# Kernel tuning notes

Measured on AMD Instinct MI355X. Metric: run time of the kernel, lower is better.

Reference implementation:

```python
import jax, jax.numpy as jnp
import numpy as np

GROUP_SIZE = 128


def setup_inputs() -> dict:
    key = jax.random.key(0)
    k0, k1, k2, k3 = jax.random.split(key, 4)
    B, S, I, O, G = 4, 2048, 4096, 11008, GROUP_SIZE
    x = jax.random.normal(k0, (B, S, I), dtype=jnp.float32)
    # int4 values in [-8, 7]
    qweight = jax.random.randint(k1, (O, I), -8, 8, dtype=jnp.int32)
    # group-wise positive scales, shape [O, I // G]
    scales = jax.random.uniform(k2, (O, I // G), dtype=jnp.float32,
                                minval=1e-3, maxval=2e-2)
    bias = jax.random.normal(k3, (O,), dtype=jnp.float32) * 0.01
    return {"x": x, "qweight": qweight, "scales": scales, "bias": bias}


def reference(x, qweight, scales, bias):
    # bits == 4, quantized path: group-wise dequant then linear
    O, I = qweight.shape
    G = GROUP_SIZE
    w = qweight.reshape(O, I // G, G).astype(x.dtype) * scales[:, :, None].astype(x.dtype)
    w = w.reshape(O, I)  # dequantized weight [O, I]
    # F.linear: y = x @ w.T + bias
    return jnp.einsum('bsi,oi->bso', x, w) + bias.astype(x.dtype)
```

## Files before the change

### kernel.cpp

```cpp
#include <hip/hip_runtime.h>
#include <hip/hip_bf16.h>


typedef __bf16 bf16_t;
typedef __bf16 bf16x8 __attribute__((ext_vector_type(8)));
typedef float f32x4 __attribute__((ext_vector_type(4)));
typedef int ix4 __attribute__((ext_vector_type(4)));
typedef __attribute__((address_space(3))) unsigned char lds_byte;
typedef __attribute__((address_space(1))) unsigned char gmem_byte;

__global__ void prep_kernel(const float* __restrict__ x, int* __restrict__ xq,
                            float* __restrict__ sx,
                            const int* __restrict__ qw, const float* __restrict__ sc,
                            float* __restrict__ tw, int* __restrict__ wq,
                            int M, int I, int NG) {
  __shared__ float red[256];
  const int b = blockIdx.x;
  const int t = threadIdx.x;
  if (b < M) {
    const float* row = x + (size_t)b * I;
    float mx = 0.f;
    for (int c = t * 4; c < I; c += 1024) {
      const float4 f = *reinterpret_cast<const float4*>(row + c);
      mx = fmaxf(mx, fmaxf(fmaxf(fabsf(f.x), fabsf(f.y)), fmaxf(fabsf(f.z), fabsf(f.w))));
    }
    red[t] = mx;
    __syncthreads();
#pragma unroll
    for (int s = 128; s > 0; s >>= 1) {
      if (t < s) red[t] = fmaxf(red[t], red[t + s]);
      __syncthreads();
    }
    const float rm = fmaxf(red[0], 1e-30f);
    if (t == 0) sx[b] = rm * (1.f / 127.f);
    const float inv = 127.f / rm;
    int* orow = xq + (size_t)b * (I >> 2);
    for (int c = t * 4; c < I; c += 1024) {
      const float4 f = *reinterpret_cast<const float4*>(row + c);
      const int b0 = (int)rintf(f.x * inv), b1 = (int)rintf(f.y * inv);
      const int b2 = (int)rintf(f.z * inv), b3 = (int)rintf(f.w * inv);
      orow[c >> 2] = (b0 & 255) | ((b1 & 255) << 8) | ((b2 & 255) << 16) | (b3 << 24);
    }
  } else {
    const int n = b - M;
    const float* srow = sc + (size_t)n * NG;
    float mx = 0.f;
    for (int g = t; g < NG; g += 256) mx = fmaxf(mx, srow[g]);
    red[t] = mx;
    __syncthreads();
#pragma unroll
    for (int s = 128; s > 0; s >>= 1) {
      if (t < s) red[t] = fmaxf(red[t], red[t + s]);
      __syncthreads();
    }
    const float tn = fmaxf(red[0], 1e-30f) * (8.f / 127.f);
    if (t == 0) tw[n] = tn;
    const float itn = 1.f / tn;
    const int* qrow = qw + (size_t)n * I;
    int* orow = wq + (size_t)n * (I >> 2);
    for (int k0 = t * 16; k0 < I; k0 += 4096) {
      const float f = srow[k0 >> 7] * itn;
      const int4* p = reinterpret_cast<const int4*>(qrow + k0);
      const int4 q0 = p[0], q1 = p[1], q2 = p[2], q3 = p[3];
      int v[16];
      v[0] = (int)rintf((float)q0.x * f); v[1] = (int)rintf((float)q0.y * f);
      v[2] = (int)rintf((float)q0.z * f); v[3] = (int)rintf((float)q0.w * f);
      v[4] = (int)rintf((float)q1.x * f); v[5] = (int)rintf((float)q1.y * f);
      v[6] = (int)rintf((float)q1.z * f); v[7] = (int)rintf((float)q1.w * f);
      v[8] = (int)rintf((float)q2.x * f); v[9] = (int)rintf((float)q2.y * f);
      v[10] = (int)rintf((float)q2.z * f); v[11] = (int)rintf((float)q2.w * f);
      v[12] = (int)rintf((float)q3.x * f); v[13] = (int)rintf((float)q3.y * f);
      v[14] = (int)rintf((float)q3.z * f); v[15] = (int)rintf((float)q3.w * f);
      int4 o;
      o.x = (v[0] & 255) | ((v[1] & 255) << 8) | ((v[2] & 255) << 16) | (v[3] << 24);
      o.y = (v[4] & 255) | ((v[5] & 255) << 8) | ((v[6] & 255) << 16) | (v[7] << 24);
      o.z = (v[8] & 255) | ((v[9] & 255) << 8) | ((v[10] & 255) << 16) | (v[11] << 24);
      o.w = (v[12] & 255) | ((v[13] & 255) << 8) | ((v[14] & 255) << 16) | (v[15] << 24);
      *reinterpret_cast<int4*>(orow + (k0 >> 2)) = o;
    }
  }
}


#define WAITV(n) asm volatile("s_waitcnt vmcnt(" #n ")" ::: "memory")
#define WAITL(n) asm volatile("s_waitcnt lgkmcnt(" #n ")" ::: "memory")
#define BAR() __builtin_amdgcn_s_barrier()
#define SETP(n) __builtin_amdgcn_s_setprio(n)

#define RD_A(DB, q) do { \
  _Pragma("unroll") \
  for (int i_ = 0; i_ < 4; ++i_) { \
    aF[i_][0] = *reinterpret_cast<const ix4*>(&ldsb[(DB) + aRd + (unsigned)((q) * 64 + i_ * 16) * 128u + ks0]); \
    aF[i_][1] = *reinterpret_cast<const ix4*>(&ldsb[(DB) + aRd + (unsigned)((q) * 64 + i_ * 16) * 128u + ks1]); \
  } \
} while (0)

#define RD_B(DB, nh, BF) do { \
  _Pragma("unroll") \
  for (int j_ = 0; j_ < 2; ++j_) { \
    BF[j_][0] = *reinterpret_cast<const ix4*>(&ldsb[(DB) + bRd + (unsigned)((nh) * 32 + j_ * 16) * 128u + ks0]); \
    BF[j_][1] = *reinterpret_cast<const ix4*>(&ldsb[(DB) + bRd + (unsigned)((nh) * 32 + j_ * 16) * 128u + ks1]); \
  } \
} while (0)

#define STG(BASE, P, tau) do { \
  __builtin_amdgcn_global_load_lds((const gmem_byte*)((P) + (size_t)(tau) * 128), \
                                   (lds_byte*)&ldsb[(BASE) + wOff], 16, 0, 0); \
  __builtin_amdgcn_global_load_lds((const gmem_byte*)((P) + (size_t)64 * K + (size_t)(tau) * 128), \
                                   (lds_byte*)&ldsb[(BASE) + 8192u + wOff], 16, 0, 0); \
} while (0)

#define MMQI(q, nh, BF) do { \
  _Pragma("unroll") \
  for (int i_ = 0; i_ < 4; ++i_) \
  _Pragma("unroll") \
  for (int j_ = 0; j_ < 2; ++j_) { \
    acc[(q) * 4 + i_][(nh) * 2 + j_] = __builtin_amdgcn_mfma_i32_16x16x64_i8(aF[i_][0], BF[j_][0], acc[(q) * 4 + i_][(nh) * 2 + j_], 0, 0, 0); \
    acc[(q) * 4 + i_][(nh) * 2 + j_] = __builtin_amdgcn_mfma_i32_16x16x64_i8(aF[i_][1], BF[j_][1], acc[(q) * 4 + i_][(nh) * 2 + j_], 0, 0, 0); \
  } \
} while (0)

__launch_bounds__(512, 2)
__global__ void gemm256_i8_kernel(const char* __restrict__ A, const char* __restrict__ B,
                                  const float* __restrict__ sx, const float* __restrict__ tw,
                                  const float* __restrict__ bias, float* __restrict__ C,
                                  int M, int N, int K) {
  __shared__ __align__(16) unsigned char ldsb[131072];

  const int tid = threadIdx.x;
  const int lane = tid & 63;
  const int w = tid >> 6;
  const int wr = w >> 2;
  const int wc = w & 3;

  const int MT = M >> 8;
  int mt, nt;
  const int bid = blockIdx.x;
  if ((MT & 7) == 0) {
    const int xcd = bid & 7, idx = bid >> 3;
    const int mpx = MT >> 3;
    nt = idx / mpx;
    mt = xcd * mpx + (idx - nt * mpx);
  } else {
    mt = bid % MT;
    nt = bid / MT;
  }
  const int m0 = mt << 8, n0 = nt << 8;

  const int srow8 = lane >> 3;
  const int scol16 = (lane & 7) ^ (srow8 & 7);
  const char* aP0 = A + (size_t)(m0 + w * 8 + srow8) * K + scol16 * 16;
  const char* aP1 = aP0 + (size_t)128 * K;
  const char* bP0 = B + (size_t)(n0 + w * 8 + srow8) * K + scol16 * 16;
  const char* bP1 = bP0 + (size_t)128 * K;
  const unsigned wOff = (unsigned)w * 1024u;

  const unsigned fr = lane & 15;
  const unsigned hi16 = (unsigned)lane >> 4;
  const unsigned sw_ = (fr & 7u) << 4;
  const unsigned ks0 = (hi16 * 16u) ^ sw_;
  const unsigned ks1 = (64u + hi16 * 16u) ^ sw_;
  const unsigned aRd = (unsigned)wr * 16384u + fr * 128u;
  const unsigned bRd = 32768u + (unsigned)(wc >> 1) * 16384u +
                       ((unsigned)(wc & 1) * 64u + fr) * 128u;

  ix4 acc[8][4];
#pragma unroll
  for (int i = 0; i < 8; ++i)
#pragma unroll
    for (int j = 0; j < 4; ++j) acc[i][j] = (ix4){0, 0, 0, 0};

  ix4 aF[4][2], bF0[2][2], bF1[2][2];

  const int NITER = K >> 8;

  STG(0u, aP0, 0); STG(16384u, aP1, 0); STG(32768u, bP0, 0); STG(49152u, bP1, 0);
  STG(98304u, bP0, 1); STG(114688u, bP1, 1);
  WAITV(4);
  BAR();

  for (int it = 0; it < NITER - 1; ++it) {
    const int t = 2 * it;
    RD_A(0u, 0); RD_B(0u, 0, bF0); RD_B(0u, 1, bF1);
    STG(65536u, aP0, t + 1); STG(81920u, aP1, t + 1);
    BAR(); WAITL(4);
    SETP(1); MMQI(0, 0, bF0); SETP(0);
    WAITL(0);
    SETP(1); MMQI(0, 1, bF1); SETP(0); BAR();
    RD_A(0u, 1);
    STG(32768u, bP0, t + 2); STG(49152u, bP1, t + 2);
    WAITV(4);
    BAR(); WAITL(0);
    SETP(1); MMQI(1, 0, bF0); MMQI(1, 1, bF1); SETP(0); BAR();
    RD_A(65536u, 0); RD_B(65536u, 0, bF0); RD_B(65536u, 1, bF1);
    STG(0u, aP0, t + 2); STG(16384u, aP1, t + 2);
    BAR(); WAITL(4);
    SETP(1); MMQI(0, 0, bF0); SETP(0);
    WAITL(0);
    SETP(1); MMQI(0, 1, bF1); SETP(0); BAR();
    RD_A(65536u, 1);
    STG(98304u, bP0, t + 3); STG(114688u, bP1, t + 3);
    WAITV(4);
    BAR(); WAITL(0);
    SETP(1); MMQI(1, 0, bF0); MMQI(1, 1, bF1); SETP(0); BAR();
  }
  {
    RD_A(0u, 0); RD_B(0u, 0, bF0); RD_B(0u, 1, bF1);
    STG(65536u, aP0, 2 * NITER - 1); STG(81920u, aP1, 2 * NITER - 1);
    BAR(); WAITL(4);
    SETP(1); MMQI(0, 0, bF0); SETP(0);
    WAITL(0);
    SETP(1); MMQI(0, 1, bF1); SETP(0); BAR();
    RD_A(0u, 1);
    WAITV(0);
    BAR(); WAITL(0);
    SETP(1); MMQI(1, 0, bF0); MMQI(1, 1, bF1); SETP(0); BAR();
    RD_A(65536u, 0); RD_B(65536u, 0, bF0); RD_B(65536u, 1, bF1);
    WAITL(4);
    SETP(1); MMQI(0, 0, bF0); SETP(0);
    WAITL(0);
    SETP(1); MMQI(0, 1, bF1); SETP(0);
    RD_A(65536u, 1);
    WAITL(0);
    SETP(1); MMQI(1, 0, bF0); MMQI(1, 1, bF1); SETP(0);
  }

  const int row0 = m0 + wr * 128 + ((lane >> 4) << 2);
  const int col0 = n0 + wc * 64 + (lane & 15);
  float sxc[8][4];
#pragma unroll
  for (int hi = 0; hi < 8; ++hi) {
    const int rbase = row0 + (hi >> 2) * 64 + (hi & 3) * 16;
#pragma unroll
    for (int r = 0; r < 4; ++r) sxc[hi][r] = sx[rbase + r];
  }
#pragma unroll
  for (int j = 0; j < 4; ++j) {
    const int n = col0 + j * 16;
    const float tn = tw[n];
    const float bv = bias[n];
#pragma unroll
    for (int hi = 0; hi < 8; ++hi) {
      const int rbase = row0 + (hi >> 2) * 64 + (hi & 3) * 16;
#pragma unroll
      for (int r = 0; r < 4; ++r)
        C[(size_t)(rbase + r) * N + n] = sxc[hi][r] * tn * (float)acc[hi][j][r] + bv;
    }
  }
}

__global__ void cvt_x_kernel(const float* __restrict__ x, bf16_t* __restrict__ xb, long n8) {
  const long stride = (long)gridDim.x * blockDim.x;
  for (long i = (long)blockIdx.x * blockDim.x + threadIdx.x; i < n8; i += stride) {
    const float4* p = reinterpret_cast<const float4*>(x + i * 8);
    const float4 f0 = p[0];
    const float4 f1 = p[1];
    bf16x8 o;
    o[0] = (bf16_t)f0.x; o[1] = (bf16_t)f0.y; o[2] = (bf16_t)f0.z; o[3] = (bf16_t)f0.w;
    o[4] = (bf16_t)f1.x; o[5] = (bf16_t)f1.y; o[6] = (bf16_t)f1.z; o[7] = (bf16_t)f1.w;
    *reinterpret_cast<bf16x8*>(xb + i * 8) = o;
  }
}

__global__ void deq_w_kernel(const int* __restrict__ qw, const float* __restrict__ sc,
                             bf16_t* __restrict__ wb, int I, int G) {
  const int n = blockIdx.y;
  const int kb = blockIdx.x * blockDim.x + threadIdx.x;
  const int k = kb * 8;
  if (k >= I) return;
  const float s = sc[(size_t)n * (I / G) + k / G];
  const int4* qp = reinterpret_cast<const int4*>(qw + (size_t)n * I + k);
  const int4 q0 = qp[0];
  const int4 q1 = qp[1];
  bf16x8 o;
  o[0] = (bf16_t)((float)q0.x * s);
  o[1] = (bf16_t)((float)q0.y * s);
  o[2] = (bf16_t)((float)q0.z * s);
  o[3] = (bf16_t)((float)q0.w * s);
  o[4] = (bf16_t)((float)q1.x * s);
  o[5] = (bf16_t)((float)q1.y * s);
  o[6] = (bf16_t)((float)q1.z * s);
  o[7] = (bf16_t)((float)q1.w * s);
  *reinterpret_cast<bf16x8*>(wb + (size_t)n * I + k) = o;
}

#define BM 128
#define BK 32
__launch_bounds__(256)
__global__ void gemm_bt_kernel(const bf16_t* __restrict__ A, const bf16_t* __restrict__ B,
                               const float* __restrict__ bias, float* __restrict__ C,
                               int M, int N, int K) {
  __shared__ __align__(16) bf16_t As[2][BM * BK];
  __shared__ __align__(16) bf16_t Bs[2][BM * BK];
  const int tid = threadIdx.x;
  const int lane = tid & 63;
  const int w = tid >> 6;
  const int wr = w >> 1;
  const int wc = w & 1;
  const int m0 = blockIdx.y * BM;
  const int n0 = blockIdx.x * BM;
  const int srow = lane >> 2;
  const int schunk = lane & 3;
  f32x4 acc[4][4];
  const f32x4 zero = {0.f, 0.f, 0.f, 0.f};
#pragma unroll
  for (int i = 0; i < 4; ++i)
#pragma unroll
    for (int j = 0; j < 4; ++j) acc[i][j] = zero;
  const int nt = K / BK;
  auto stage = [&](int t, int buf) {
    const int k0 = t * BK;
#pragma unroll
    for (int j = 0; j < 2; ++j) {
      const int row = w * 32 + j * 16;
      const bf16_t* ga = A + (size_t)(m0 + row + srow) * K + k0 + schunk * 8;
      __builtin_amdgcn_global_load_lds((const gmem_byte*)ga, (lds_byte*)&As[buf][row * BK], 16, 0, 0);
      const bf16_t* gb = B + (size_t)(n0 + row + srow) * K + k0 + schunk * 8;
      __builtin_amdgcn_global_load_lds((const gmem_byte*)gb, (lds_byte*)&Bs[buf][row * BK], 16, 0, 0);
    }
  };
  auto compute = [&](int buf) {
    bf16x8 af[4], bfr[4];
    const int fr2 = lane & 15;
    const int kc = (lane >> 4) * 8;
#pragma unroll
    for (int i = 0; i < 4; ++i) {
      af[i] = *reinterpret_cast<const bf16x8*>(&As[buf][(wr * 64 + i * 16 + fr2) * BK + kc]);
      bfr[i] = *reinterpret_cast<const bf16x8*>(&Bs[buf][(wc * 64 + i * 16 + fr2) * BK + kc]);
    }
#pragma unroll
    for (int i = 0; i < 4; ++i)
#pragma unroll
      for (int j = 0; j < 4; ++j)
        acc[i][j] = __builtin_amdgcn_mfma_f32_16x16x32_bf16(af[i], bfr[j], acc[i][j], 0, 0, 0);
  };
  stage(0, 0);
  __syncthreads();
  int cur = 0;
  for (int t = 0; t < nt - 1; ++t) {
    stage(t + 1, cur ^ 1);
    compute(cur);
    __syncthreads();
    cur ^= 1;
  }
  compute(cur);
#pragma unroll
  for (int j = 0; j < 4; ++j) {
    const int n = n0 + wc * 64 + j * 16 + (lane & 15);
    const float bv = bias[n];
#pragma unroll
    for (int i = 0; i < 4; ++i) {
      const int mbase = m0 + wr * 64 + i * 16 + (lane >> 4) * 4;
#pragma unroll
      for (int r = 0; r < 4; ++r)
        C[(size_t)(mbase + r) * N + n] = acc[i][j][r] + bv;
    }
  }
}

extern "C" void kernel_launch(void* const* d_in, const int* in_sizes, int n_in,
                              void* d_out, int out_size, void* d_ws, size_t ws_size,
                              hipStream_t stream) {
  const float* x = (const float*)d_in[0];
  const int* qw = (const int*)d_in[1];
  const float* sc = (const float*)d_in[2];
  const float* bias = (const float*)d_in[3];
  float* out = (float*)d_out;

  const long O = in_sizes[3];
  const long I = in_sizes[1] / O;
  const long M = in_sizes[0] / I;
  const long G = I / (in_sizes[2] / O);
  const long NG = I / G;

  const size_t i8need = (size_t)(M + O) * I + 4 * (size_t)(M + O);
  const bool i8ok = ((M & 255) == 0) && ((O & 255) == 0) && ((I & 255) == 0) &&
                    (G == 128) && ((I >> 8) >= 2) &&
                    (ws_size >= i8need);
  if (i8ok) {
    char* xq = (char*)d_ws;
    char* wq = xq + (size_t)M * I;
    float* sx = (float*)(wq + (size_t)O * I);
    float* tw = sx + M;
    prep_kernel<<<(unsigned)(M + O), 256, 0, stream>>>(x, (int*)xq, sx, qw, sc, tw,
                                                       (int*)wq, (int)M, (int)I, (int)NG);
    const int nwg = (int)((M >> 8) * (O >> 8));
    gemm256_i8_kernel<<<nwg, 512, 0, stream>>>(xq, wq, sx, tw, bias, out, (int)M, (int)O, (int)I);
  } else {
    bf16_t* xb = (bf16_t*)d_ws;
    bf16_t* wb = xb + (size_t)M * I;
    if (ws_size < (size_t)(M + O) * I * sizeof(bf16_t)) return;
    cvt_x_kernel<<<2048, 256, 0, stream>>>(x, xb, M * I / 8);
    dim3 dgrid((unsigned)((I / 8 + 255) / 256), (unsigned)O);
    deq_w_kernel<<<dgrid, 256, 0, stream>>>(qw, sc, wb, (int)I, (int)G);
    dim3 ggrid((unsigned)(O / BM), (unsigned)(M / BM));
    gemm_bt_kernel<<<ggrid, 256, 0, stream>>>(xb, wb, bias, out, (int)M, (int)O, (int)I);
  }
}
```

Before: 487.3 us.

## Shrink int8 GEMM tile to 128x128 with simpler double-buffered pipeline

Replaces the 256x256 output tile int8 MFMA GEMM with a 128x128 tile. Each of 8 waves now computes 32x64, LDS drops to 64KB, and launch bounds allow 4 blocks per CU. The staged split-phase schedule becomes a plain two-buffer ping-pong over 128-wide K chunks. This aims to raise occupancy and simplify synchronisation, but it lowers arithmetic intensity per LDS read and global load.

```diff
diff --git a/kernel.cpp b/kernel.cpp
--- a/kernel.cpp
+++ b/kernel.cpp
@@ -87,19 +87,16 @@
 #define BAR() __builtin_amdgcn_s_barrier()
 #define SETP(n) __builtin_amdgcn_s_setprio(n)
 
-#define RD_A(DB, q) do { \
+#define RD_T(DB) do { \
   _Pragma("unroll") \
-  for (int i_ = 0; i_ < 4; ++i_) { \
-    aF[i_][0] = *reinterpret_cast<const ix4*>(&ldsb[(DB) + aRd + (unsigned)((q) * 64 + i_ * 16) * 128u + ks0]); \
-    aF[i_][1] = *reinterpret_cast<const ix4*>(&ldsb[(DB) + aRd + (unsigned)((q) * 64 + i_ * 16) * 128u + ks1]); \
+  for (int m_ = 0; m_ < 2; ++m_) { \
+    aF[m_][0] = *reinterpret_cast<const ix4*>(&ldsb[(DB) + aRd + (unsigned)(m_ * 16) * 128u + ks0]); \
+    aF[m_][1] = *reinterpret_cast<const ix4*>(&ldsb[(DB) + aRd + (unsigned)(m_ * 16) * 128u + ks1]); \
   } \
-} while (0)
-
-#define RD_B(DB, nh, BF) do { \
   _Pragma("unroll") \
-  for (int j_ = 0; j_ < 2; ++j_) { \
-    BF[j_][0] = *reinterpret_cast<const ix4*>(&ldsb[(DB) + bRd + (unsigned)((nh) * 32 + j_ * 16) * 128u + ks0]); \
-    BF[j_][1] = *reinterpret_cast<const ix4*>(&ldsb[(DB) + bRd + (unsigned)((nh) * 32 + j_ * 16) * 128u + ks1]); \
+  for (int n_ = 0; n_ < 4; ++n_) { \
+    bF[n_][0] = *reinterpret_cast<const ix4*>(&ldsb[(DB) + 16384u + bRd + (unsigned)(n_ * 16) * 128u + ks0]); \
+    bF[n_][1] = *reinterpret_cast<const ix4*>(&ldsb[(DB) + 16384u + bRd + (unsigned)(n_ * 16) * 128u + ks1]); \
   } \
 } while (0)
 
@@ -110,30 +107,30 @@
                                    (lds_byte*)&ldsb[(BASE) + 8192u + wOff], 16, 0, 0); \
 } while (0)
 
-#define MMQI(q, nh, BF) do { \
+#define MM_T() do { \
   _Pragma("unroll") \
-  for (int i_ = 0; i_ < 4; ++i_) \
+  for (int m_ = 0; m_ < 2; ++m_) \
   _Pragma("unroll") \
-  for (int j_ = 0; j_ < 2; ++j_) { \
-    acc[(q) * 4 + i_][(nh) * 2 + j_] = __builtin_amdgcn_mfma_i32_16x16x64_i8(aF[i_][0], BF[j_][0], acc[(q) * 4 + i_][(nh) * 2 + j_], 0, 0, 0); \
-    acc[(q) * 4 + i_][(nh) * 2 + j_] = __builtin_amdgcn_mfma_i32_16x16x64_i8(aF[i_][1], BF[j_][1], acc[(q) * 4 + i_][(nh) * 2 + j_], 0, 0, 0); \
+  for (int n_ = 0; n_ < 4; ++n_) { \
+    acc[m_][n_] = __builtin_amdgcn_mfma_i32_16x16x64_i8(aF[m_][0], bF[n_][0], acc[m_][n_], 0, 0, 0); \
+    acc[m_][n_] = __builtin_amdgcn_mfma_i32_16x16x64_i8(aF[m_][1], bF[n_][1], acc[m_][n_], 0, 0, 0); \
   } \
 } while (0)
 
-__launch_bounds__(512, 2)
-__global__ void gemm256_i8_kernel(const char* __restrict__ A, const char* __restrict__ B,
+__launch_bounds__(512, 4)
+__global__ void gemm128_i8_kernel(const char* __restrict__ A, const char* __restrict__ B,
                                   const float* __restrict__ sx, const float* __restrict__ tw,
                                   const float* __restrict__ bias, float* __restrict__ C,
                                   int M, int N, int K) {
-  __shared__ __align__(16) unsigned char ldsb[131072];
+  __shared__ __align__(16) unsigned char ldsb[65536];
 
   const int tid = threadIdx.x;
   const int lane = tid & 63;
   const int w = tid >> 6;
-  const int wr = w >> 2;
-  const int wc = w & 3;
-
-  const int MT = M >> 8;
+  const int wr = w >> 1;
+  const int wc = w & 1;
+
+  const int MT = M >> 7;
   int mt, nt;
   const int bid = blockIdx.x;
   if ((MT & 7) == 0) {
@@ -145,14 +142,12 @@
     mt = bid % MT;
     nt = bid / MT;
   }
-  const int m0 = mt << 8, n0 = nt << 8;
+  const int m0 = mt << 7, n0 = nt << 7;
 
   const int srow8 = lane >> 3;
   const int scol16 = (lane & 7) ^ (srow8 & 7);
-  const char* aP0 = A + (size_t)(m0 + w * 8 + srow8) * K + scol16 * 16;
-  const char* aP1 = aP0 + (size_t)128 * K;
-  const char* bP0 = B + (size_t)(n0 + w * 8 + srow8) * K + scol16 * 16;
-  const char* bP1 = bP0 + (size_t)128 * K;
+  const char* aP = A + (size_t)(m0 + w * 8 + srow8) * K + scol16 * 16;
+  const char* bP = B + (size_t)(n0 + w * 8 + srow8) * K + scol16 * 16;
   const unsigned wOff = (unsigned)w * 1024u;
 
   const unsigned fr = lane & 15;
@@ -160,91 +155,72 @@
   const unsigned sw_ = (fr & 7u) << 4;
   const unsigned ks0 = (hi16 * 16u) ^ sw_;
   const unsigned ks1 = (64u + hi16 * 16u) ^ sw_;
-  const unsigned aRd = (unsigned)wr * 16384u + fr * 128u;
-  const unsigned bRd = 32768u + (unsigned)(wc >> 1) * 16384u +
-                       ((unsigned)(wc & 1) * 64u + fr) * 128u;
-
-  ix4 acc[8][4];
-#pragma unroll
-  for (int i = 0; i < 8; ++i)
+  const unsigned aRd = ((unsigned)(wr * 32) + fr) * 128u;
+  const unsigned bRd = ((unsigned)(wc * 64) + fr) * 128u;
+
+  ix4 acc[2][4];
+#pragma unroll
+  for (int i = 0; i < 2; ++i)
 #pragma unroll
     for (int j = 0; j < 4; ++j) acc[i][j] = (ix4){0, 0, 0, 0};
 
-  ix4 aF[4][2], bF0[2][2], bF1[2][2];
-
-  const int NITER = K >> 8;
-
-  STG(0u, aP0, 0); STG(16384u, aP1, 0); STG(32768u, bP0, 0); STG(49152u, bP1, 0);
-  STG(98304u, bP0, 1); STG(114688u, bP1, 1);
+  ix4 aF[2][2], bF[4][2];
+
+  const int NITER = K >> 7;
+
+  STG(0u, aP, 0); STG(16384u, bP, 0);
+  STG(32768u, aP, 1); STG(49152u, bP, 1);
   WAITV(4);
   BAR();
 
-  for (int it = 0; it < NITER - 1; ++it) {
+  for (int it = 0; it < (NITER >> 1) - 1; ++it) {
     const int t = 2 * it;
-    RD_A(0u, 0); RD_B(0u, 0, bF0); RD_B(0u, 1, bF1);
-    STG(65536u, aP0, t + 1); STG(81920u, aP1, t + 1);
-    BAR(); WAITL(4);
-    SETP(1); MMQI(0, 0, bF0); SETP(0);
+    RD_T(0u);
     WAITL(0);
-    SETP(1); MMQI(0, 1, bF1); SETP(0); BAR();
-    RD_A(0u, 1);
-    STG(32768u, bP0, t + 2); STG(49152u, bP1, t + 2);
+    BAR();
+    STG(0u, aP, t + 2); STG(16384u, bP, t + 2);
+    SETP(1); MM_T(); SETP(0);
     WAITV(4);
-    BAR(); WAITL(0);
-    SETP(1); MMQI(1, 0, bF0); MMQI(1, 1, bF1); SETP(0); BAR();
-    RD_A(65536u, 0); RD_B(65536u, 0, bF0); RD_B(65536u, 1, bF1);
-    STG(0u, aP0, t + 2); STG(16384u, aP1, t + 2);
-    BAR(); WAITL(4);
-    SETP(1); MMQI(0, 0, bF0); SETP(0);
+    BAR();
+    RD_T(32768u);
     WAITL(0);
-    SETP(1); MMQI(0, 1, bF1); SETP(0); BAR();
-    RD_A(65536u, 1);
-    STG(98304u, bP0, t + 3); STG(114688u, bP1, t + 3);
+    BAR();
+    STG(32768u, aP, t + 3); STG(49152u, bP, t + 3);
+    SETP(1); MM_T(); SETP(0);
     WAITV(4);
-    BAR(); WAITL(0);
-    SETP(1); MMQI(1, 0, bF0); MMQI(1, 1, bF1); SETP(0); BAR();
+    BAR();
   }
   {
-    RD_A(0u, 0); RD_B(0u, 0, bF0); RD_B(0u, 1, bF1);
-    STG(65536u, aP0, 2 * NITER - 1); STG(81920u, aP1, 2 * NITER - 1);
-    BAR(); WAITL(4);
-    SETP(1); MMQI(0, 0, bF0); SETP(0);
+    RD_T(0u);
+    WAITV(0);
+    BAR();
     WAITL(0);
-    SETP(1); MMQI(0, 1, bF1); SETP(0); BAR();
-    RD_A(0u, 1);
-    WAITV(0);
-    BAR(); WAITL(0);
-    SETP(1); MMQI(1, 0, bF0); MMQI(1, 1, bF1); SETP(0); BAR();
-    RD_A(65536u, 0); RD_B(65536u, 0, bF0); RD_B(65536u, 1, bF1);
-    WAITL(4);
-    SETP(1); MMQI(0, 0, bF0); SETP(0);
+    SETP(1); MM_T(); SETP(0);
+    RD_T(32768u);
     WAITL(0);
-    SETP(1); MMQI(0, 1, bF1); SETP(0);
-    RD_A(65536u, 1);
-    WAITL(0);
-    SETP(1); MMQI(1, 0, bF0); MMQI(1, 1, bF1); SETP(0);
-  }
-
-  const int row0 = m0 + wr * 128 + ((lane >> 4) << 2);
+    SETP(1); MM_T(); SETP(0);
+  }
+
+  const int row0 = m0 + wr * 32 + ((lane >> 4) << 2);
   const int col0 = n0 + wc * 64 + (lane & 15);
-  float sxc[8][4];
-#pragma unroll
-  for (int hi = 0; hi < 8; ++hi) {
-    const int rbase = row0 + (hi >> 2) * 64 + (hi & 3) * 16;
-#pragma unroll
-    for (int r = 0; r < 4; ++r) sxc[hi][r] = sx[rbase + r];
-  }
-#pragma unroll
-  for (int j = 0; j < 4; ++j) {
-    const int n = col0 + j * 16;
+  float sxc[2][4];
+#pragma unroll
+  for (int m_ = 0; m_ < 2; ++m_) {
+    const int rbase = row0 + m_ * 16;
+#pragma unroll
+    for (int r = 0; r < 4; ++r) sxc[m_][r] = sx[rbase + r];
+  }
+#pragma unroll
+  for (int n_ = 0; n_ < 4; ++n_) {
+    const int n = col0 + n_ * 16;
     const float tn = tw[n];
     const float bv = bias[n];
 #pragma unroll
-    for (int hi = 0; hi < 8; ++hi) {
-      const int rbase = row0 + (hi >> 2) * 64 + (hi & 3) * 16;
+    for (int m_ = 0; m_ < 2; ++m_) {
+      const int rbase = row0 + m_ * 16;
 #pragma unroll
       for (int r = 0; r < 4; ++r)
-        C[(size_t)(rbase + r) * N + n] = sxc[hi][r] * tn * (float)acc[hi][j][r] + bv;
+        C[(size_t)(rbase + r) * N + n] = sxc[m_][r] * tn * (float)acc[m_][n_][r] + bv;
     }
   }
 }
@@ -374,8 +350,9 @@
   const long NG = I / G;
 
   const size_t i8need = (size_t)(M + O) * I + 4 * (size_t)(M + O);
-  const bool i8ok = ((M & 255) == 0) && ((O & 255) == 0) && ((I & 255) == 0) &&
-                    (G == 128) && ((I >> 8) >= 2) &&
+  const long NITER = I >> 7;
+  const bool i8ok = ((M & 127) == 0) && ((O & 127) == 0) && ((I & 127) == 0) &&
+                    (G == 128) && (NITER >= 4) && ((NITER & 1) == 0) &&
                     (ws_size >= i8need);
   if (i8ok) {
     char* xq = (char*)d_ws;
@@ -384,8 +361,8 @@
     float* tw = sx + M;
     prep_kernel<<<(unsigned)(M + O), 256, 0, stream>>>(x, (int*)xq, sx, qw, sc, tw,
                                                        (int*)wq, (int)M, (int)I, (int)NG);
-    const int nwg = (int)((M >> 8) * (O >> 8));
-    gemm256_i8_kernel<<<nwg, 512, 0, stream>>>(xq, wq, sx, tw, bias, out, (int)M, (int)O, (int)I);
+    const int nwg = (int)((M >> 7) * (O >> 7));
+    gemm128_i8_kernel<<<nwg, 512, 0, stream>>>(xq, wq, sx, tw, bias, out, (int)M, (int)O, (int)I);
   } else {
     bf16_t* xb = (bf16_t*)d_ws;
     bf16_t* wb = xb + (size_t)M * I;
```

After: 483.1 us, median of 3. About the same (-0.9%).
